# Performance work log

Measured on AMD Instinct MI355X. Metric: run time of the kernel, lower is better.

The kernel has to match this reference:

```python
import jax, jax.numpy as jnp
import numpy as np

N = 50000   # nodes
E = 300000  # edges
D = 256     # emb_dim
L = 5       # num_layers
BN_EPS = 1e-5


def setup_inputs() -> dict:
    key = jax.random.key(0)
    ks = jax.random.split(key, 6)
    scale = 0.05
    return {
        "x": jax.random.normal(ks[0], (N, D), jnp.float32),
        "src": jax.random.randint(ks[1], (E,), 0, N, dtype=jnp.int32),
        "dst": jax.random.randint(ks[2], (E,), 0, N, dtype=jnp.int32),
        "W1": jax.random.normal(ks[3], (L, D, D), jnp.float32) * scale,
        "b1": jnp.zeros((L, D), jnp.float32),
        "g1": jnp.ones((L, D), jnp.float32),
        "bt1": jnp.zeros((L, D), jnp.float32),
        "W2": jax.random.normal(ks[4], (L, D, D), jnp.float32) * scale,
        "b2": jnp.zeros((L, D), jnp.float32),
        "eps": jnp.zeros((L,), jnp.float32),
        "bn_g": jnp.ones((L, D), jnp.float32),
        "bn_b": jnp.zeros((L, D), jnp.float32),
    }


def _bn(h, gamma, beta):
    # torch BatchNorm1d training-mode forward: biased batch stats over nodes
    mean = jnp.mean(h, axis=0)
    var = jnp.var(h, axis=0)
    return (h - mean) * jax.lax.rsqrt(var + BN_EPS) * gamma + beta


def reference(x, src, dst, W1, b1, g1, bt1, W2, b2, eps, bn_g, bn_b):
    h = x
    for l in range(L):
        # GINConv: gather relu(x[src]) -> scatter-sum to dst
        msg = jax.nn.relu(h[src])                          # [E, D]
        agg = jax.ops.segment_sum(msg, dst, num_segments=N)  # [N, D]
        z = (1.0 + eps[l]) * h + agg
        # mlp: Linear -> BN -> ReLU -> Linear
        z = z @ W1[l] + b1[l]
        z = jax.nn.relu(_bn(z, g1[l], bt1[l]))
        z = z @ W2[l] + b2[l]
        # per-layer BatchNorm; dropout is identity (eval / drop_ratio=0)
        z = _bn(z, bn_g[l], bn_b[l])
        if l < L - 1:
            z = jax.nn.relu(z)
        h = z
    return h  # JK='last'
```

## Files before the change

### kernel.cpp

```cpp
#include <hip/hip_runtime.h>
#include <hip/hip_bf16.h>

#define N_NODES 50000
#define N_EDGES 300000
#define DIM 256
#define MPAD 50048

typedef __attribute__((ext_vector_type(8))) _Float16 half8;
typedef __attribute__((ext_vector_type(4))) _Float16 half4;
typedef __attribute__((ext_vector_type(4))) float f32x4;

__device__ __forceinline__ void async16(const void* g, void* l) {
    __builtin_amdgcn_global_load_lds(
        (const __attribute__((address_space(1))) unsigned int*)g,
        (__attribute__((address_space(3))) unsigned int*)l, 16, 0, 0);
}

__global__ __launch_bounds__(256) void hist_dst(const int* __restrict__ dst,
                                                int* __restrict__ deg, int E) {
    int e = blockIdx.x * blockDim.x + threadIdx.x;
    if (e < E) atomicAdd(&deg[dst[e]], 1);
}

__global__ __launch_bounds__(1024) void scan_blk(const int* __restrict__ deg,
                                                 int* __restrict__ ptr,
                                                 int* __restrict__ bsum, int n) {
    __shared__ int wsum[16];
    __shared__ int wpre[16];
    int tid = threadIdx.x;
    int i = blockIdx.x * 1024 + tid;
    int v = (i < n) ? deg[i] : 0;
    int lane = tid & 63, w = tid >> 6;
    int s = v;
#pragma unroll
    for (int off = 1; off < 64; off <<= 1) {
        int t = __shfl_up(s, off, 64);
        if (lane >= off) s += t;
    }
    if (lane == 63) wsum[w] = s;
    __syncthreads();
    if (tid < 16) {
        int acc = 0;
        for (int j = 0; j < tid; j++) acc += wsum[j];
        wpre[tid] = acc;
    }
    __syncthreads();
    int incl = s + wpre[w];
    if (i < n) ptr[i] = incl - v;
    if (tid == 1023) bsum[blockIdx.x] = incl;
}

__global__ __launch_bounds__(64) void scan_top(int* __restrict__ bsum,
                                               int* __restrict__ ptr,
                                               int nb, int n, int E) {
    int lane = threadIdx.x;
    int v = (lane < nb) ? bsum[lane] : 0;
    int s = v;
#pragma unroll
    for (int off = 1; off < 64; off <<= 1) {
        int t = __shfl_up(s, off, 64);
        if (lane >= off) s += t;
    }
    if (lane < nb) bsum[lane] = s - v;
    if (lane == 0) ptr[n] = E;
}

__global__ __launch_bounds__(1024) void scan_add(int* __restrict__ ptr,
                                                 const int* __restrict__ bsum,
                                                 int* __restrict__ cursor, int n) {
    int i = blockIdx.x * 1024 + threadIdx.x;
    if (i < n) {
        int val = ptr[i] + bsum[blockIdx.x];
        ptr[i] = val;
        cursor[i] = val;
    }
}

__global__ __launch_bounds__(256) void scatter_src(const int* __restrict__ src,
                                                   const int* __restrict__ dst,
                                                   int* __restrict__ cursor,
                                                   int* __restrict__ srcbuf, int E) {
    int e = blockIdx.x * blockDim.x + threadIdx.x;
    if (e < E) {
        int pos = atomicAdd(&cursor[dst[e]], 1);
        srcbuf[pos] = src[e];
    }
}

__global__ __launch_bounds__(256) void x2h(const float* __restrict__ x,
                                           _Float16* __restrict__ hb) {
    size_t i = (size_t)blockIdx.x * 256 + threadIdx.x;
    float4 v = ((const float4*)x)[i];
    half4 o;
    o.x = (_Float16)v.x; o.y = (_Float16)v.y;
    o.z = (_Float16)v.z; o.w = (_Float16)v.w;
    ((half4*)hb)[i] = o;
}

__global__ __launch_bounds__(256) void wconv(const float* __restrict__ W1,
                                             const float* __restrict__ W2,
                                             _Float16* __restrict__ Wt) {
    int mat = blockIdx.x >> 4;
    int t = blockIdx.x & 15;
    int tr = t >> 2, tc = t & 3;
    const float* W = (mat < 5) ? (W1 + (size_t)mat * 65536)
                               : (W2 + (size_t)(mat - 5) * 65536);
    __shared__ float tile[64][65];
    int tid = threadIdx.x;
    int c = tid & 63, r0 = tid >> 6;
#pragma unroll 4
    for (int i = 0; i < 16; i++) {
        int r = r0 + i * 4;
        tile[r][c] = W[(size_t)(tr * 64 + r) * 256 + tc * 64 + c];
    }
    __syncthreads();
    _Float16* o = Wt + (size_t)mat * 65536;
#pragma unroll 4
    for (int i = 0; i < 16; i++) {
        int r = r0 + i * 4;
        o[(size_t)(tc * 64 + r) * 256 + tr * 64 + c] = (_Float16)tile[c][r];
    }
}

__global__ __launch_bounds__(256) void gather_h(const _Float16* __restrict__ h,
                                                const int* __restrict__ ptr,
                                                const int* __restrict__ srcbuf,
                                                _Float16* __restrict__ z,
                                                const float* __restrict__ eps) {
    int node = blockIdx.x * 4 + (threadIdx.x >> 6);
    if (node >= N_NODES) return;
    int lane = threadIdx.x & 63;
    int beg = ptr[node], end = ptr[node + 1];
    float s = 1.0f + eps[0];
    half4 hv = ((const half4*)(h + (size_t)node * DIM))[lane];
    float a0 = (float)hv.x * s, a1 = (float)hv.y * s;
    float a2 = (float)hv.z * s, a3 = (float)hv.w * s;
    int e = beg;
    for (; e + 4 <= end; e += 4) {
        int s0 = srcbuf[e], s1 = srcbuf[e + 1], s2 = srcbuf[e + 2], s3 = srcbuf[e + 3];
        half4 v0 = ((const half4*)(h + (size_t)s0 * DIM))[lane];
        half4 v1 = ((const half4*)(h + (size_t)s1 * DIM))[lane];
        half4 v2 = ((const half4*)(h + (size_t)s2 * DIM))[lane];
        half4 v3 = ((const half4*)(h + (size_t)s3 * DIM))[lane];
        a0 += fmaxf((float)v0.x, 0.f) + fmaxf((float)v1.x, 0.f)
            + fmaxf((float)v2.x, 0.f) + fmaxf((float)v3.x, 0.f);
        a1 += fmaxf((float)v0.y, 0.f) + fmaxf((float)v1.y, 0.f)
            + fmaxf((float)v2.y, 0.f) + fmaxf((float)v3.y, 0.f);
        a2 += fmaxf((float)v0.z, 0.f) + fmaxf((float)v1.z, 0.f)
            + fmaxf((float)v2.z, 0.f) + fmaxf((float)v3.z, 0.f);
        a3 += fmaxf((float)v0.w, 0.f) + fmaxf((float)v1.w, 0.f)
            + fmaxf((float)v2.w, 0.f) + fmaxf((float)v3.w, 0.f);
    }
    for (; e < end; e++) {
        half4 v = ((const half4*)(h + (size_t)srcbuf[e] * DIM))[lane];
        a0 += fmaxf((float)v.x, 0.f); a1 += fmaxf((float)v.y, 0.f);
        a2 += fmaxf((float)v.z, 0.f); a3 += fmaxf((float)v.w, 0.f);
    }
    half4 o;
    o.x = (_Float16)a0; o.y = (_Float16)a1;
    o.z = (_Float16)a2; o.w = (_Float16)a3;
    ((half4*)(z + (size_t)node * DIM))[lane] = o;
}

__global__ __launch_bounds__(256) void gather_bn(const _Float16* __restrict__ C,
                                                 const int* __restrict__ ptr,
                                                 const int* __restrict__ srcbuf,
                                                 _Float16* __restrict__ z,
                                                 const float* __restrict__ scsh,
                                                 const float* __restrict__ eps,
                                                 int l) {
    int node = blockIdx.x * 4 + (threadIdx.x >> 6);
    if (node >= N_NODES) return;
    int lane = threadIdx.x & 63;
    float4 sc = ((const float4*)scsh)[lane];
    float4 sh = ((const float4*)(scsh + DIM))[lane];
    int beg = ptr[node], end = ptr[node + 1];
    float s = 1.0f + eps[l];
    half4 hv = ((const half4*)(C + (size_t)node * DIM))[lane];
    float a0 = s * fmaxf((float)hv.x * sc.x + sh.x, 0.f);
    float a1 = s * fmaxf((float)hv.y * sc.y + sh.y, 0.f);
    float a2 = s * fmaxf((float)hv.z * sc.z + sh.z, 0.f);
    float a3 = s * fmaxf((float)hv.w * sc.w + sh.w, 0.f);
    int e = beg;
    for (; e + 4 <= end; e += 4) {
        int s0 = srcbuf[e], s1 = srcbuf[e + 1], s2 = srcbuf[e + 2], s3 = srcbuf[e + 3];
        half4 v0 = ((const half4*)(C + (size_t)s0 * DIM))[lane];
        half4 v1 = ((const half4*)(C + (size_t)s1 * DIM))[lane];
        half4 v2 = ((const half4*)(C + (size_t)s2 * DIM))[lane];
        half4 v3 = ((const half4*)(C + (size_t)s3 * DIM))[lane];
        a0 += fmaxf((float)v0.x * sc.x + sh.x, 0.f) + fmaxf((float)v1.x * sc.x + sh.x, 0.f)
            + fmaxf((float)v2.x * sc.x + sh.x, 0.f) + fmaxf((float)v3.x * sc.x + sh.x, 0.f);
        a1 += fmaxf((float)v0.y * sc.y + sh.y, 0.f) + fmaxf((float)v1.y * sc.y + sh.y, 0.f)
            + fmaxf((float)v2.y * sc.y + sh.y, 0.f) + fmaxf((float)v3.y * sc.y + sh.y, 0.f);
        a2 += fmaxf((float)v0.z * sc.z + sh.z, 0.f) + fmaxf((float)v1.z * sc.z + sh.z, 0.f)
            + fmaxf((float)v2.z * sc.z + sh.z, 0.f) + fmaxf((float)v3.z * sc.z + sh.z, 0.f);
        a3 += fmaxf((float)v0.w * sc.w + sh.w, 0.f) + fmaxf((float)v1.w * sc.w + sh.w, 0.f)
            + fmaxf((float)v2.w * sc.w + sh.w, 0.f) + fmaxf((float)v3.w * sc.w + sh.w, 0.f);
    }
    for (; e < end; e++) {
        half4 v = ((const half4*)(C + (size_t)srcbuf[e] * DIM))[lane];
        a0 += fmaxf((float)v.x * sc.x + sh.x, 0.f);
        a1 += fmaxf((float)v.y * sc.y + sh.y, 0.f);
        a2 += fmaxf((float)v.z * sc.z + sh.z, 0.f);
        a3 += fmaxf((float)v.w * sc.w + sh.w, 0.f);
    }
    half4 o;
    o.x = (_Float16)a0; o.y = (_Float16)a1;
    o.z = (_Float16)a2; o.w = (_Float16)a3;
    ((half4*)(z + (size_t)node * DIM))[lane] = o;
}

#define GEMM_EPILOGUE                                                        \
    __syncthreads();                                                         \
    float* colsum = (float*)((char*)smem + 49152);                           \
    float* colsq = colsum + 128;                                             \
    if (tid < 128) { colsum[tid] = 0.0f; colsq[tid] = 0.0f; }                \
    _Float16* Cs = (_Float16*)smem;                                          \
    float bcol[4];                                                           \
    _Pragma("unroll")                                                        \
    for (int j = 0; j < 4; j++) bcol[j] = bias[col0 + wn + j * 16 + lrow];   \
    float csum[4] = {0.f, 0.f, 0.f, 0.f};                                    \
    float csq[4] = {0.f, 0.f, 0.f, 0.f};                                     \
    _Pragma("unroll")                                                        \
    for (int i = 0; i < 4; i++) {                                            \
        int rl = wm + i * 16 + quad * 4;                                     \
        _Pragma("unroll")                                                    \
        for (int j = 0; j < 4; j++) {                                        \
            int cl = wn + j * 16 + lrow;                                     \
            _Pragma("unroll")                                                \
            for (int r = 0; r < 4; r++) {                                    \
                float v = acc[i][j][r] + bcol[j];                            \
                Cs[(rl + r) * 136 + cl] = (_Float16)v;                       \
                if (row0 + rl + r < M) { csum[j] += v; csq[j] += v * v; }    \
            }                                                                \
        }                                                                    \
    }                                                                        \
    __syncthreads();                                                         \
    {                                                                        \
        int rgrp = lane >> 4, ch = lane & 15;                                \
        _Pragma("unroll")                                                    \
        for (int it = 0; it < 8; it++) {                                     \
            int row = wid * 32 + it * 4 + rgrp;                              \
            uint4 vv = *(const uint4*)(Cs + row * 136 + ch * 8);             \
            *(uint4*)(C + (size_t)(row0 + row) * DIM + col0 + ch * 8) = vv;  \
        }                                                                    \
    }                                                                        \
    _Pragma("unroll")                                                        \
    for (int j = 0; j < 4; j++) {                                            \
        atomicAdd(&colsum[wn + j * 16 + lrow], csum[j]);                     \
        atomicAdd(&colsq[wn + j * 16 + lrow], csq[j]);                       \
    }                                                                        \
    __syncthreads();                                                         \
    if (tid < 128) {                                                         \
        float* st = stats + (blockIdx.y & 7) * 512;                          \
        atomicAdd(&st[col0 + tid], colsum[tid]);                             \
        atomicAdd(&st[DIM + col0 + tid], colsq[tid]);                        \
    }

__global__ __launch_bounds__(256) void gemm_f16(const _Float16* __restrict__ A,
                                                const _Float16* __restrict__ Wt,
                                                const float* __restrict__ bias,
                                                _Float16* __restrict__ C,
                                                float* __restrict__ stats,
                                                int M) {
    __shared__ uint4 smem[4096];

    int tid = threadIdx.x;
    int wid = tid >> 6, lane = tid & 63;
    int quad = lane >> 4, lrow = lane & 15;
    int row0 = blockIdx.y * 128, col0 = blockIdx.x * 128;
    int wm = (wid & 1) * 64, wn = (wid >> 1) * 64;

    f32x4 acc[4][4] = {};
    const char* Ab = (const char*)A;
    const char* Bb = (const char*)Wt;

#pragma unroll
    for (int ko = 0; ko < 2; ko++) {
        int kb0 = ko * 256;
#pragma unroll
        for (int j = 0; j < 8; j++) {
            int sbase = wid * 512 + j * 64;
            int s = sbase + lane;
            int m = s >> 4;
            int c = (s & 15) ^ (m & 7);
            size_t go = (size_t)(row0 + m) * 512 + kb0 + c * 16;
            async16(Ab + go, (char*)smem + sbase * 16);
            size_t gob = (size_t)(col0 + m) * 512 + kb0 + c * 16;
            async16(Bb + gob, (char*)smem + 32768 + sbase * 16);
        }
        __syncthreads();
#pragma unroll
        for (int kc = 0; kc < 4; kc++) {
            half8 af[4], bf[4];
#pragma unroll
            for (int t = 0; t < 4; t++) {
                int ma = wm + t * 16 + lrow;
                int ca = kc * 4 + quad;
                af[t] = *(const half8*)((const char*)smem +
                                        (ma * 16 + (ca ^ (ma & 7))) * 16);
                int mb = wn + t * 16 + lrow;
                bf[t] = *(const half8*)((const char*)smem + 32768 +
                                        (mb * 16 + (ca ^ (mb & 7))) * 16);
            }
#pragma unroll
            for (int i = 0; i < 4; i++)
#pragma unroll
                for (int j2 = 0; j2 < 4; j2++)
                    acc[i][j2] = __builtin_amdgcn_mfma_f32_16x16x32_f16(
                        af[i], bf[j2], acc[i][j2], 0, 0, 0);
        }
        if (ko == 0) __syncthreads();
    }

    GEMM_EPILOGUE
}

__global__ __launch_bounds__(256) void gemm_bn(const _Float16* __restrict__ A,
                                               const _Float16* __restrict__ Wt,
                                               const float* __restrict__ bias,
                                               const float* __restrict__ scsh,
                                               _Float16* __restrict__ C,
                                               float* __restrict__ stats,
                                               int M) {
    __shared__ uint4 smem[4096];

    int tid = threadIdx.x;
    int wid = tid >> 6, lane = tid & 63;
    int quad = lane >> 4, lrow = lane & 15;
    int row0 = blockIdx.y * 128, col0 = blockIdx.x * 128;
    int wm = (wid & 1) * 64, wn = (wid >> 1) * 64;

    half8 scv[8], shv[8];
#pragma unroll
    for (int cc = 0; cc < 8; cc++) {
        int kk = cc * 32 + quad * 8;
        float4 s0 = *(const float4*)(scsh + kk);
        float4 s1 = *(const float4*)(scsh + kk + 4);
        float4 h0 = *(const float4*)(scsh + DIM + kk);
        float4 h1 = *(const float4*)(scsh + DIM + kk + 4);
        half8 sv = {(_Float16)s0.x, (_Float16)s0.y, (_Float16)s0.z, (_Float16)s0.w,
                    (_Float16)s1.x, (_Float16)s1.y, (_Float16)s1.z, (_Float16)s1.w};
        half8 hv = {(_Float16)h0.x, (_Float16)h0.y, (_Float16)h0.z, (_Float16)h0.w,
                    (_Float16)h1.x, (_Float16)h1.y, (_Float16)h1.z, (_Float16)h1.w};
        scv[cc] = sv;
        shv[cc] = hv;
    }

    f32x4 acc[4][4] = {};
    const char* Ab = (const char*)A;
    const char* Bb = (const char*)Wt;
    const half8 zerov = {0, 0, 0, 0, 0, 0, 0, 0};

#pragma unroll
    for (int ko = 0; ko < 2; ko++) {
        int kb0 = ko * 256;
#pragma unroll
        for (int j = 0; j < 8; j++) {
            int sbase = wid * 512 + j * 64;
            int s = sbase + lane;
            int m = s >> 4;
            int c = (s & 15) ^ (m & 7);
            size_t go = (size_t)(row0 + m) * 512 + kb0 + c * 16;
            async16(Ab + go, (char*)smem + sbase * 16);
            size_t gob = (size_t)(col0 + m) * 512 + kb0 + c * 16;
            async16(Bb + gob, (char*)smem + 32768 + sbase * 16);
        }
        __syncthreads();
#pragma unroll
        for (int kc = 0; kc < 4; kc++) {
            half8 af[4], bf[4];
            half8 sv = scv[ko * 4 + kc];
            half8 hv = shv[ko * 4 + kc];
#pragma unroll
            for (int t = 0; t < 4; t++) {
                int ma = wm + t * 16 + lrow;
                int ca = kc * 4 + quad;
                half8 a = *(const half8*)((const char*)smem +
                                          (ma * 16 + (ca ^ (ma & 7))) * 16);
                af[t] = __builtin_elementwise_max(a * sv + hv, zerov);
                int mb = wn + t * 16 + lrow;
                bf[t] = *(const half8*)((const char*)smem + 32768 +
                                        (mb * 16 + (ca ^ (mb & 7))) * 16);
            }
#pragma unroll
            for (int i = 0; i < 4; i++)
#pragma unroll
                for (int j2 = 0; j2 < 4; j2++)
                    acc[i][j2] = __builtin_amdgcn_mfma_f32_16x16x32_f16(
                        af[i], bf[j2], acc[i][j2], 0, 0, 0);
        }
        if (ko == 0) __syncthreads();
    }

    GEMM_EPILOGUE
}

__global__ __launch_bounds__(256) void bn_finalize(float* __restrict__ stats,
                                                   const float* __restrict__ g,
                                                   const float* __restrict__ beta,
                                                   float* __restrict__ scsh,
                                                   int n) {
    int d = threadIdx.x;
    float s = 0.0f, sq = 0.0f;
#pragma unroll
    for (int r = 0; r < 8; r++) {
        s += stats[r * 512 + d];
        sq += stats[r * 512 + 256 + d];
        stats[r * 512 + d] = 0.0f;
        stats[r * 512 + 256 + d] = 0.0f;
    }
    float invn = 1.0f / (float)n;
    float mean = s * invn;
    float var = sq * invn - mean * mean;
    float inv = rsqrtf(var + 1e-5f);
    float scale = g[d] * inv;
    scsh[d] = scale;
    scsh[DIM + d] = beta[d] - mean * scale;
}

__global__ __launch_bounds__(256) void bn_apply_f(const _Float16* __restrict__ in,
                                                  float* __restrict__ outf,
                                                  const float* __restrict__ scsh) {
    size_t i = (size_t)blockIdx.x * 256 + threadIdx.x;
    int c4 = (int)(i & 63);
    float4 sc = ((const float4*)scsh)[c4];
    float4 sh = ((const float4*)(scsh + DIM))[c4];
    half4 v = ((const half4*)in)[i];
    float4 o;
    o.x = (float)v.x * sc.x + sh.x;
    o.y = (float)v.y * sc.y + sh.y;
    o.z = (float)v.z * sc.z + sh.z;
    o.w = (float)v.w * sc.w + sh.w;
    ((float4*)outf)[i] = o;
}

extern "C" void kernel_launch(void* const* d_in, const int* in_sizes, int n_in,
                              void* d_out, int out_size, void* d_ws, size_t ws_size,
                              hipStream_t stream) {
    (void)in_sizes; (void)n_in; (void)out_size; (void)ws_size;
    const float* x   = (const float*)d_in[0];
    const int*   src = (const int*)d_in[1];
    const int*   dst = (const int*)d_in[2];
    const float* W1  = (const float*)d_in[3];
    const float* b1  = (const float*)d_in[4];
    const float* g1  = (const float*)d_in[5];
    const float* bt1 = (const float*)d_in[6];
    const float* W2  = (const float*)d_in[7];
    const float* b2  = (const float*)d_in[8];
    const float* eps = (const float*)d_in[9];
    const float* bng = (const float*)d_in[10];
    const float* bnb = (const float*)d_in[11];
    float* out = (float*)d_out;

    const int N = N_NODES, E = N_EDGES, D = DIM;
    size_t NDp = (size_t)MPAD * D;

    _Float16* gin  = (_Float16*)d_ws;
    _Float16* C1   = gin + NDp;
    _Float16* C2   = C1 + NDp;
    _Float16* Wt   = C2 + NDp;
    float* statsA = (float*)(Wt + 10 * 65536);
    float* statsB = statsA + 4096;
    float* scshA = statsB + 4096;
    float* scshB = scshA + 512;
    int* deg     = (int*)(scshB + 512);
    int* ptr     = deg + N;
    int* bsum    = ptr + N + 1;
    int* srcbuf  = bsum + 64;

    const int ELEM4_BLOCKS = N * D / 4 / 256;
    const int NODE_BLOCKS  = (N + 3) / 4;
    const int E_BLOCKS     = (E + 255) / 256;
    const int SCAN_BLOCKS  = (N + 1023) / 1024;
    const dim3 GEMM_GRID(2, MPAD / 128);

    hipMemsetAsync(deg, 0, N * sizeof(int), stream);
    hipMemsetAsync(statsA, 0, 8192 * sizeof(float), stream);
    hist_dst<<<E_BLOCKS, 256, 0, stream>>>(dst, deg, E);
    scan_blk<<<SCAN_BLOCKS, 1024, 0, stream>>>(deg, ptr, bsum, N);
    scan_top<<<1, 64, 0, stream>>>(bsum, ptr, SCAN_BLOCKS, N, E);
    scan_add<<<SCAN_BLOCKS, 1024, 0, stream>>>(ptr, bsum, deg, N);
    scatter_src<<<E_BLOCKS, 256, 0, stream>>>(src, dst, deg, srcbuf, E);
    wconv<<<160, 256, 0, stream>>>(W1, W2, Wt);
    x2h<<<ELEM4_BLOCKS, 256, 0, stream>>>(x, C1);

    for (int l = 0; l < 5; l++) {
        if (l == 0)
            gather_h<<<NODE_BLOCKS, 256, 0, stream>>>(C1, ptr, srcbuf, gin, eps);
        else
            gather_bn<<<NODE_BLOCKS, 256, 0, stream>>>(C2, ptr, srcbuf, gin,
                                                       scshB, eps, l);

        gemm_f16<<<GEMM_GRID, 256, 0, stream>>>(
            gin, Wt + (size_t)l * 65536, b1 + (size_t)l * D, C1, statsA, N);
        bn_finalize<<<1, 256, 0, stream>>>(statsA, g1 + (size_t)l * D,
                                           bt1 + (size_t)l * D, scshA, N);

        gemm_bn<<<GEMM_GRID, 256, 0, stream>>>(
            C1, Wt + (size_t)(5 + l) * 65536, b2 + (size_t)l * D, scshA,
            C2, statsB, N);
        bn_finalize<<<1, 256, 0, stream>>>(statsB, bng + (size_t)l * D,
                                           bnb + (size_t)l * D, scshB, N);

        if (l == 4)
            bn_apply_f<<<ELEM4_BLOCKS, 256, 0, stream>>>(C2, out, scshB);
    }
}
```

Before: 661.7 us.

## Load full-K A tile to LDS, read weights from global, spread BN stat atomics

Both GEMM kernels now load the whole 128x256 A tile into LDS in one pass and read the weight fragments directly from global memory (cached) instead of staging them in LDS. This removes one barrier and the two-phase K loop. __launch_bounds__(256,2) is added to encourage two blocks per CU. BN statistics atomics are spread over 32 partial slots instead of 8, which reduces contention. Each GEMM gets its own pre-zeroed stats buffer, so bn_finalize no longer has to re-zero it. The risk is that the direct global weight loads may add latency to the MFMA loop.

```diff
diff --git a/kernel.cpp b/kernel.cpp
--- a/kernel.cpp
+++ b/kernel.cpp
@@ -252,17 +252,17 @@
     }                                                                        \
     __syncthreads();                                                         \
     if (tid < 128) {                                                         \
-        float* st = stats + (blockIdx.y & 7) * 512;                          \
+        float* st = stats + (blockIdx.y & 31) * 512;                         \
         atomicAdd(&st[col0 + tid], colsum[tid]);                             \
         atomicAdd(&st[DIM + col0 + tid], colsq[tid]);                        \
     }
 
-__global__ __launch_bounds__(256) void gemm_f16(const _Float16* __restrict__ A,
-                                                const _Float16* __restrict__ Wt,
-                                                const float* __restrict__ bias,
-                                                _Float16* __restrict__ C,
-                                                float* __restrict__ stats,
-                                                int M) {
+__global__ __launch_bounds__(256, 2) void gemm_f16(const _Float16* __restrict__ A,
+                                                   const _Float16* __restrict__ Wt,
+                                                   const float* __restrict__ bias,
+                                                   _Float16* __restrict__ C,
+                                                   float* __restrict__ stats,
+                                                   int M) {
     __shared__ uint4 smem[4096];
 
     int tid = threadIdx.x;
@@ -271,58 +271,50 @@
     int row0 = blockIdx.y * 128, col0 = blockIdx.x * 128;
     int wm = (wid & 1) * 64, wn = (wid >> 1) * 64;
 
+    const char* Ab = (const char*)A;
+#pragma unroll
+    for (int j = 0; j < 16; j++) {
+        int sbase = wid * 1024 + j * 64;
+        int s = sbase + lane;
+        int m = s >> 5;
+        int cg = (s & 31) ^ (m & 7);
+        async16(Ab + (size_t)(row0 + m) * 512 + cg * 16,
+                (char*)smem + sbase * 16);
+    }
+
     f32x4 acc[4][4] = {};
-    const char* Ab = (const char*)A;
-    const char* Bb = (const char*)Wt;
-
-#pragma unroll
-    for (int ko = 0; ko < 2; ko++) {
-        int kb0 = ko * 256;
-#pragma unroll
-        for (int j = 0; j < 8; j++) {
-            int sbase = wid * 512 + j * 64;
-            int s = sbase + lane;
-            int m = s >> 4;
-            int c = (s & 15) ^ (m & 7);
-            size_t go = (size_t)(row0 + m) * 512 + kb0 + c * 16;
-            async16(Ab + go, (char*)smem + sbase * 16);
-            size_t gob = (size_t)(col0 + m) * 512 + kb0 + c * 16;
-            async16(Bb + gob, (char*)smem + 32768 + sbase * 16);
+    __syncthreads();
+
+#pragma unroll
+    for (int kc = 0; kc < 8; kc++) {
+        half8 af[4], bf[4];
+#pragma unroll
+        for (int t = 0; t < 4; t++) {
+            int ma = wm + t * 16 + lrow;
+            int ca = kc * 4 + quad;
+            af[t] = *(const half8*)((const char*)smem +
+                                    (ma * 32 + (ca ^ (ma & 7))) * 16);
+            bf[t] = *(const half8*)(Wt + (size_t)(col0 + wn + t * 16 + lrow) * 256 +
+                                    kc * 32 + quad * 8);
         }
-        __syncthreads();
-#pragma unroll
-        for (int kc = 0; kc < 4; kc++) {
-            half8 af[4], bf[4];
-#pragma unroll
-            for (int t = 0; t < 4; t++) {
-                int ma = wm + t * 16 + lrow;
-                int ca = kc * 4 + quad;
-                af[t] = *(const half8*)((const char*)smem +
-                                        (ma * 16 + (ca ^ (ma & 7))) * 16);
-                int mb = wn + t * 16 + lrow;
-                bf[t] = *(const half8*)((const char*)smem + 32768 +
-                                        (mb * 16 + (ca ^ (mb & 7))) * 16);
-            }
-#pragma unroll
-            for (int i = 0; i < 4; i++)
-#pragma unroll
-                for (int j2 = 0; j2 < 4; j2++)
-                    acc[i][j2] = __builtin_amdgcn_mfma_f32_16x16x32_f16(
-                        af[i], bf[j2], acc[i][j2], 0, 0, 0);
-        }
-        if (ko == 0) __syncthreads();
+#pragma unroll
+        for (int i = 0; i < 4; i++)
+#pragma unroll
+            for (int j2 = 0; j2 < 4; j2++)
+                acc[i][j2] = __builtin_amdgcn_mfma_f32_16x16x32_f16(
+                    af[i], bf[j2], acc[i][j2], 0, 0, 0);
     }
 
     GEMM_EPILOGUE
 }
 
-__global__ __launch_bounds__(256) void gemm_bn(const _Float16* __restrict__ A,
-                                               const _Float16* __restrict__ Wt,
-                                               const float* __restrict__ bias,
-                                               const float* __restrict__ scsh,
-                                               _Float16* __restrict__ C,
-                                               float* __restrict__ stats,
-                                               int M) {
+__global__ __launch_bounds__(256, 2) void gemm_bn(const _Float16* __restrict__ A,
+                                                  const _Float16* __restrict__ Wt,
+                                                  const float* __restrict__ bias,
+                                                  const float* __restrict__ scsh,
+                                                  _Float16* __restrict__ C,
+                                                  float* __restrict__ stats,
+                                                  int M) {
     __shared__ uint4 smem[4096];
 
     int tid = threadIdx.x;
@@ -330,6 +322,17 @@
     int quad = lane >> 4, lrow = lane & 15;
     int row0 = blockIdx.y * 128, col0 = blockIdx.x * 128;
     int wm = (wid & 1) * 64, wn = (wid >> 1) * 64;
+
+    const char* Ab = (const char*)A;
+#pragma unroll
+    for (int j = 0; j < 16; j++) {
+        int sbase = wid * 1024 + j * 64;
+        int s = sbase + lane;
+        int m = s >> 5;
+        int cg = (s & 31) ^ (m & 7);
+        async16(Ab + (size_t)(row0 + m) * 512 + cg * 16,
+                (char*)smem + sbase * 16);
+    }
 
     half8 scv[8], shv[8];
 #pragma unroll
@@ -348,67 +351,46 @@
     }
 
     f32x4 acc[4][4] = {};
-    const char* Ab = (const char*)A;
-    const char* Bb = (const char*)Wt;
     const half8 zerov = {0, 0, 0, 0, 0, 0, 0, 0};
-
-#pragma unroll
-    for (int ko = 0; ko < 2; ko++) {
-        int kb0 = ko * 256;
-#pragma unroll
-        for (int j = 0; j < 8; j++) {
-            int sbase = wid * 512 + j * 64;
-            int s = sbase + lane;
-            int m = s >> 4;
-            int c = (s & 15) ^ (m & 7);
-            size_t go = (size_t)(row0 + m) * 512 + kb0 + c * 16;
-            async16(Ab + go, (char*)smem + sbase * 16);
-            size_t gob = (size_t)(col0 + m) * 512 + kb0 + c * 16;
-            async16(Bb + gob, (char*)smem + 32768 + sbase * 16);
+    __syncthreads();
+
+#pragma unroll
+    for (int kc = 0; kc < 8; kc++) {
+        half8 af[4], bf[4];
+        half8 sv = scv[kc];
+        half8 hv = shv[kc];
+#pragma unroll
+        for (int t = 0; t < 4; t++) {
+            int ma = wm + t * 16 + lrow;
+            int ca = kc * 4 + quad;
+            half8 a = *(const half8*)((const char*)smem +
+                                      (ma * 32 + (ca ^ (ma & 7))) * 16);
+            af[t] = __builtin_elementwise_max(a * sv + hv, zerov);
+            bf[t] = *(const half8*)(Wt + (size_t)(col0 + wn + t * 16 + lrow) * 256 +
+                                    kc * 32 + quad * 8);
         }
-        __syncthreads();
-#pragma unroll
-        for (int kc = 0; kc < 4; kc++) {
-            half8 af[4], bf[4];
-            half8 sv = scv[ko * 4 + kc];
-            half8 hv = shv[ko * 4 + kc];
-#pragma unroll
-            for (int t = 0; t < 4; t++) {
-                int ma = wm + t * 16 + lrow;
-                int ca = kc * 4 + quad;
-                half8 a = *(const half8*)((const char*)smem +
-                                          (ma * 16 + (ca ^ (ma & 7))) * 16);
-                af[t] = __builtin_elementwise_max(a * sv + hv, zerov);
-                int mb = wn + t * 16 + lrow;
-                bf[t] = *(const half8*)((const char*)smem + 32768 +
-                                        (mb * 16 + (ca ^ (mb & 7))) * 16);
-            }
-#pragma unroll
-            for (int i = 0; i < 4; i++)
-#pragma unroll
-                for (int j2 = 0; j2 < 4; j2++)
-                    acc[i][j2] = __builtin_amdgcn_mfma_f32_16x16x32_f16(
-                        af[i], bf[j2], acc[i][j2], 0, 0, 0);
-        }
-        if (ko == 0) __syncthreads();
+#pragma unroll
+        for (int i = 0; i < 4; i++)
+#pragma unroll
+            for (int j2 = 0; j2 < 4; j2++)
+                acc[i][j2] = __builtin_amdgcn_mfma_f32_16x16x32_f16(
+                    af[i], bf[j2], acc[i][j2], 0, 0, 0);
     }
 
     GEMM_EPILOGUE
 }
 
-__global__ __launch_bounds__(256) void bn_finalize(float* __restrict__ stats,
+__global__ __launch_bounds__(256) void bn_finalize(const float* __restrict__ stats,
                                                    const float* __restrict__ g,
                                                    const float* __restrict__ beta,
                                                    float* __restrict__ scsh,
                                                    int n) {
     int d = threadIdx.x;
     float s = 0.0f, sq = 0.0f;
-#pragma unroll
-    for (int r = 0; r < 8; r++) {
+#pragma unroll 8
+    for (int r = 0; r < 32; r++) {
         s += stats[r * 512 + d];
         sq += stats[r * 512 + 256 + d];
-        stats[r * 512 + d] = 0.0f;
-        stats[r * 512 + 256 + d] = 0.0f;
     }
     float invn = 1.0f / (float)n;
     float mean = s * invn;
@@ -460,9 +442,8 @@
     _Float16* C1   = gin + NDp;
     _Float16* C2   = C1 + NDp;
     _Float16* Wt   = C2 + NDp;
-    float* statsA = (float*)(Wt + 10 * 65536);
-    float* statsB = statsA + 4096;
-    float* scshA = statsB + 4096;
+    float* statsG = (float*)(Wt + 10 * 65536);
+    float* scshA = statsG + 10 * 32 * 512;
     float* scshB = scshA + 512;
     int* deg     = (int*)(scshB + 512);
     int* ptr     = deg + N;
@@ -476,7 +457,7 @@
     const dim3 GEMM_GRID(2, MPAD / 128);
 
     hipMemsetAsync(deg, 0, N * sizeof(int), stream);
-    hipMemsetAsync(statsA, 0, 8192 * sizeof(float), stream);
+    hipMemsetAsync(statsG, 0, 10 * 32 * 512 * sizeof(float), stream);
     hist_dst<<<E_BLOCKS, 256, 0, stream>>>(dst, deg, E);
     scan_blk<<<SCAN_BLOCKS, 1024, 0, stream>>>(deg, ptr, bsum, N);
     scan_top<<<1, 64, 0, stream>>>(bsum, ptr, SCAN_BLOCKS, N, E);
@@ -486,6 +467,9 @@
     x2h<<<ELEM4_BLOCKS, 256, 0, stream>>>(x, C1);
 
     for (int l = 0; l < 5; l++) {
+        float* stA = statsG + (size_t)(l * 2) * 32 * 512;
+        float* stB = statsG + (size_t)(l * 2 + 1) * 32 * 512;
+
         if (l == 0)
             gather_h<<<NODE_BLOCKS, 256, 0, stream>>>(C1, ptr, srcbuf, gin, eps);
         else
@@ -493,14 +477,14 @@
                                                        scshB, eps, l);
 
         gemm_f16<<<GEMM_GRID, 256, 0, stream>>>(
-            gin, Wt + (size_t)l * 65536, b1 + (size_t)l * D, C1, statsA, N);
-        bn_finalize<<<1, 256, 0, stream>>>(statsA, g1 + (size_t)l * D,
+            gin, Wt + (size_t)l * 65536, b1 + (size_t)l * D, C1, stA, N);
+        bn_finalize<<<1, 256, 0, stream>>>(stA, g1 + (size_t)l * D,
                                            bt1 + (size_t)l * D, scshA, N);
 
         gemm_bn<<<GEMM_GRID, 256, 0, stream>>>(
             C1, Wt + (size_t)(5 + l) * 65536, b2 + (size_t)l * D, scshA,
-            C2, statsB, N);
-        bn_finalize<<<1, 256, 0, stream>>>(statsB, bng + (size_t)l * D,
+            C2, stB, N);
+        bn_finalize<<<1, 256, 0, stream>>>(stB, bng + (size_t)l * D,
                                            bnb + (size_t)l * D, scshB, N);
 
         if (l == 4)
```

Measured after the change: 736.4 us. 11.3% more time.
